# Optimization experiments

Hardware: AMD Instinct MI355X
Metric: run time of the kernel (lower is better)

## Reference

```python
import jax, jax.numpy as jnp
import numpy as np

QMIN, QMAX = -128, 127  # signed int8 range


def setup_inputs() -> dict:
    key = jax.random.key(0)
    k_x, k_w, k_b = jax.random.split(key, 3)
    N, C_in, H, W = 32, 128, 56, 56
    C_out, kH, kW = 256, 3, 3
    # int8-valued tensors carried as int32 (jax-friendly); values in [-128, 127]
    x = jax.random.randint(k_x, (N, C_in, H, W), 0, 256, dtype=jnp.int32) - 128
    weight = jax.random.randint(k_w, (C_out, C_in, kH, kW), 0, 256, dtype=jnp.int32) - 128
    # int32 bias, already quantized with scale s_in * s_w
    bias = jax.random.randint(k_b, (C_out,), -(2 ** 14), 2 ** 14, dtype=jnp.int32)
    return {
        "x": x,
        "weight": weight,
        "bias": bias,
        "input_scale": jnp.float32(0.02),
        "weight_scale": jnp.float32(0.005),
        "output_scale": jnp.float32(0.05),
        "input_zero_point": jnp.int32(-5),
        "output_zero_point": jnp.int32(3),
    }


def reference(x, weight, bias, input_scale, weight_scale, output_scale,
              input_zero_point, output_zero_point):
    # Dequant-style integer conv: shift input by its zero point (weights are
    # symmetric, zero point 0), accumulate in fp32 (stands in for int32 acc).
    x_f = (x - input_zero_point).astype(jnp.float32)
    w_f = weight.astype(jnp.float32)
    acc = jax.lax.conv_general_dilated(
        x_f, w_f,
        window_strides=(1, 1),
        padding=((1, 1), (1, 1)),
        dimension_numbers=("NCHW", "OIHW", "NCHW"),
    )
    acc = acc + bias.astype(jnp.float32)[None, :, None, None]
    # Requantize: scale fusion + output zero point, round, clamp to int8.
    requant_scale = input_scale * weight_scale / output_scale
    y = acc * requant_scale + output_zero_point.astype(jnp.float32)
    y_q = jnp.clip(jnp.round(y), QMIN, QMAX).astype(jnp.int8)
    return y_q
```

## Files before the change

kernel.cpp:

```cpp
#include <hip/hip_runtime.h>
#include <stdint.h>


#define NB 32
#define CI 128
#define HH 56
#define WW 56
#define CO 256
#define SPA (HH * WW)
#define HP 58
#define WP 64
#define XP2_BYTES (NB * HP * WP * CI)
#define BP_BYTES (9 * 2 * 4 * CO * 16)

typedef int v4i __attribute__((ext_vector_type(4)));

__global__ __launch_bounds__(256) void prep_kernel(
    const int* __restrict__ x, const int* __restrict__ wgt,
    const int* __restrict__ bias, const int* __restrict__ zpi,
    int8_t* __restrict__ xp2, int8_t* __restrict__ bp, int* __restrict__ BG)
{
    __shared__ int sm[1824];
    const int tid = threadIdx.x, bid = blockIdx.x;
    const int zp = *zpi;
    const int zp4 = (zp & 255) * 0x01010101;

    if (bid < HH * NB) {
        const int n = bid / HH, h = bid % HH;
        #pragma unroll
        for (int it = 0; it < 7; ++it) {
            int j = tid + it * 256;
            int ci = j / 14, w4 = j - ci * 14;
            const v4i v = *(const v4i*)(x + ((n * CI + ci) * HH + h) * WW + w4 * 4);
            sm[w4 * 130 + ci] = (v.x & 255) | ((v.y & 255) << 8) |
                                ((v.z & 255) << 16) | (v.w << 24);
        }
        __syncthreads();
        int* od = (int*)xp2 + (n * HP + h + 1) * (WP * CI / 4);
        #pragma unroll
        for (int it = 0; it < 8; ++it) {
            int j = tid + it * 256;
            int widx = j >> 5, ci4 = j & 31;
            int val = zp4;
            if (widx >= 1 && widx <= WW) {
                int w = widx - 1;
                int base = (w >> 2) * 130 + ci4 * 4;
                int sh = (w & 3) * 8;
                val = ((sm[base] >> sh) & 0xff) | (((sm[base+1] >> sh) & 0xff) << 8) |
                      (((sm[base+2] >> sh) & 0xff) << 16) | ((sm[base+3] >> sh) << 24);
            }
            od[j ^ ((widx & 7) << 2)] = val;
        }
    } else if (bid < HH * NB + 2 * NB) {
        const int z = bid - HH * NB;
        const int n = z >> 1, hidx = (z & 1) ? (HP - 1) : 0;
        int* od = (int*)xp2 + (n * HP + hidx) * (WP * CI / 4);
        #pragma unroll
        for (int it = 0; it < 8; ++it) od[tid + it * 256] = zp4;
    } else {
        const int co = bid - (HH * NB + 2 * NB);
        for (int j = tid; j < 1152; j += 256) sm[j] = wgt[co * 1152 + j];
        __syncthreads();
        for (int j = tid; j < 288; j += 256) {
            int j4 = j & 3, q = (j >> 2) & 3, c64 = (j >> 4) & 1, t = j >> 5;
            int ci = c64 * 64 + q * 16 + j4 * 4;
            int b0 = sm[(ci + 0) * 9 + t] & 255, b1 = sm[(ci + 1) * 9 + t] & 255;
            int b2 = sm[(ci + 2) * 9 + t] & 255, b3 = sm[(ci + 3) * 9 + t];
            ((int*)bp)[((t * 2 + c64) * 4 + q) * 1024 + co * 4 + j4] =
                b0 | (b1 << 8) | (b2 << 16) | (b3 << 24);
        }
        if (tid < 9) {
            int s = 0;
            for (int ci = 0; ci < CI; ++ci) s += sm[ci * 9 + tid];
            sm[1152 + tid] = s;
        }
        __syncthreads();
        if (tid == 0) {
            int s9 = 0;
            for (int t = 0; t < 9; ++t) s9 += sm[1152 + t];
            BG[co] = bias[co] - zp * s9;
        }
    }
}

__global__ __launch_bounds__(256, 1) void qconv_mfma(
    const int8_t* __restrict__ xp2, const int8_t* __restrict__ bp,
    const int* __restrict__ BG,
    const float* __restrict__ si, const float* __restrict__ sw,
    const float* __restrict__ so, const int* __restrict__ zpo,
    int* __restrict__ out)
{
    const int tid  = threadIdx.x, lane = tid & 63, wid = tid >> 6;
    const int quad = lane >> 4, lo16 = lane & 15;
    const int bid  = blockIdx.x;
    const int xcd  = bid & 7, idx = bid >> 3;
    const int co64 = idx & 3, slab = idx >> 2;
    const int gslab = xcd * 28 + slab;
    const int n = gslab / 7, blk8 = gslab % 7;
    const int cobase = co64 * 64;
    const int p0   = blk8 * 8;
    const int remS = blk8 * 448;

    __shared__ __attribute__((aligned(16))) char smem[152 * 1024];
    char* Asm = smem;
    char* Bsm = smem + 80 * 1024;

    const int8_t* aslab = xp2 + (((size_t)n * HP + p0) << 13);
    #pragma unroll
    for (int k = 0; k < 20; ++k) {
        const int u = wid + 4 * k;
        __builtin_amdgcn_global_load_lds(
            (const __attribute__((address_space(1))) void*)(aslab + (u << 10) + lane * 16),
            (__attribute__((address_space(3))) void*)(Asm + (u << 10)), 16, 0, 0);
    }
    #pragma unroll
    for (int k = 0; k < 18; ++k) {
        const int u = wid + 4 * k;
        __builtin_amdgcn_global_load_lds(
            (const __attribute__((address_space(1))) void*)(bp + (u << 12) + cobase * 16 + lane * 16),
            (__attribute__((address_space(3))) void*)(Bsm + (u << 10)), 16, 0, 0);
    }

    int abase[7];
    const int mw = wid * 112;
    #pragma unroll
    for (int mt = 0; mt < 7; ++mt) {
        const int ml = mw + mt * 16 + lo16;
        const int srow = ml / 56, scol = ml - srow * 56;
        abase[mt] = (srow * WP + scol) * 128 + quad * 16;
    }

    int bgv[4];
    #pragma unroll
    for (int ct = 0; ct < 4; ++ct) bgv[ct] = BG[cobase + ct * 16 + lo16];
    const float rs = (*si) * (*sw) / (*so);
    const float zo = (float)(*zpo);

    v4i acc[7][4];
    #pragma unroll
    for (int mt = 0; mt < 7; ++mt)
        #pragma unroll
        for (int ct = 0; ct < 4; ++ct) acc[mt][ct] = (v4i){0, 0, 0, 0};

    __syncthreads();

    #pragma unroll
    for (int t = 0; t < 9; ++t) {
        const int toff = ((t / 3) * WP + (t % 3)) * 128;
        v4i b[2][4];
        #pragma unroll
        for (int c = 0; c < 2; ++c)
            #pragma unroll
            for (int ct = 0; ct < 4; ++ct)
                b[c][ct] = *(const v4i*)(Bsm + ((t * 2 + c) * 4 + quad) * 1024 +
                                         lo16 * 16 + ct * 256);
        #pragma unroll
        for (int mt = 0; mt < 7; ++mt) {
            const int P = abase[mt] + toff;
            const int phys = P ^ (((P >> 7) & 7) << 4);
            v4i a0 = *(const v4i*)(Asm + phys);
            v4i a1 = *(const v4i*)(Asm + (phys ^ 64));
            #pragma unroll
            for (int ct = 0; ct < 4; ++ct)
                acc[mt][ct] = __builtin_amdgcn_mfma_i32_16x16x64_i8(a0, b[0][ct], acc[mt][ct], 0, 0, 0);
            #pragma unroll
            for (int ct = 0; ct < 4; ++ct)
                acc[mt][ct] = __builtin_amdgcn_mfma_i32_16x16x64_i8(a1, b[1][ct], acc[mt][ct], 0, 0, 0);
        }
    }

    __syncthreads();
    int* lt = (int*)smem + wid * 1088;

    #pragma unroll
    for (int mt = 0; mt < 7; ++mt) {
        #pragma unroll
        for (int ct = 0; ct < 4; ++ct) {
            v4i vv;
            #pragma unroll
            for (int i = 0; i < 4; ++i) {
                float y = rintf((float)(acc[mt][ct][i] + bgv[ct]) * rs + zo);
                y = fminf(fmaxf(y, -128.f), 127.f);
                vv[i] = (int)y;
            }
            *(v4i*)(lt + (ct * 16 + lo16) * 17 + quad * 4) = vv;
        }
        const int rm0 = remS + mw + mt * 16;
        #pragma unroll
        for (int it = 0; it < 4; ++it) {
            const int col = it * 16 + (lane >> 2);
            const int m4  = (lane & 3) * 4;
            v4i v = *(const v4i*)(lt + col * 17 + m4);
            *(v4i*)(out + ((n * CO + cobase + col) * SPA + rm0 + m4)) = v;
        }
    }
}

extern "C" void kernel_launch(void* const* d_in, const int* in_sizes, int n_in,
                              void* d_out, int out_size, void* d_ws, size_t ws_size,
                              hipStream_t stream) {
    const int*   x    = (const int*)d_in[0];
    const int*   wgt  = (const int*)d_in[1];
    const int*   bias = (const int*)d_in[2];
    const float* si   = (const float*)d_in[3];
    const float* sw   = (const float*)d_in[4];
    const float* so   = (const float*)d_in[5];
    const int*   zpi  = (const int*)d_in[6];
    const int*   zpo  = (const int*)d_in[7];
    int* out = (int*)d_out;

    int8_t* xp2 = (int8_t*)d_ws;
    int8_t* bp  = xp2 + XP2_BYTES;
    int*    bg  = (int*)(bp + BP_BYTES);

    prep_kernel<<<HH * NB + 2 * NB + CO, 256, 0, stream>>>(x, wgt, bias, zpi, xp2, bp, bg);
    qconv_mfma<<<896, 256, 0, stream>>>(xp2, bp, bg, si, sw, so, zpo, out);
}
```

Before: 202.0 us.

## Make conv blocks persistent over row slabs with register-prefetched next A tile

The grid shrinks from 896 to 256 blocks, one per CU. Each block keeps its weight tile in LDS and loops over 3 or 4 row slabs of one image and 64-channel group. The next slab's activations are prefetched into registers during the MFMA loop and written to LDS after a barrier. The epilogue stores requantized results straight to global memory instead of transposing through LDS. This amortizes the weight load and launch cost and overlaps activation loads with compute, at the cost of heavy register pressure (20 prefetch vectors plus 28 accumulators), extra barriers, and less coalesced output stores.

```diff
diff --git a/kernel.cpp b/kernel.cpp
--- a/kernel.cpp
+++ b/kernel.cpp
@@ -93,26 +93,18 @@
     const int tid  = threadIdx.x, lane = tid & 63, wid = tid >> 6;
     const int quad = lane >> 4, lo16 = lane & 15;
     const int bid  = blockIdx.x;
-    const int xcd  = bid & 7, idx = bid >> 3;
-    const int co64 = idx & 3, slab = idx >> 2;
-    const int gslab = xcd * 28 + slab;
-    const int n = gslab / 7, blk8 = gslab % 7;
+    const int x    = bid & 7, yb = bid >> 3;
+    const int half = yb >> 4, coli = yb & 15;
+    const int col  = x * 16 + coli;
+    const int n = col >> 2, co64 = col & 3;
     const int cobase = co64 * 64;
-    const int p0   = blk8 * 8;
-    const int remS = blk8 * 448;
+    const int sfirst = half;
+    const int ntiles = half ? 3 : 4;
 
     __shared__ __attribute__((aligned(16))) char smem[152 * 1024];
     char* Asm = smem;
     char* Bsm = smem + 80 * 1024;
 
-    const int8_t* aslab = xp2 + (((size_t)n * HP + p0) << 13);
-    #pragma unroll
-    for (int k = 0; k < 20; ++k) {
-        const int u = wid + 4 * k;
-        __builtin_amdgcn_global_load_lds(
-            (const __attribute__((address_space(1))) void*)(aslab + (u << 10) + lane * 16),
-            (__attribute__((address_space(3))) void*)(Asm + (u << 10)), 16, 0, 0);
-    }
     #pragma unroll
     for (int k = 0; k < 18; ++k) {
         const int u = wid + 4 * k;
@@ -120,6 +112,14 @@
             (const __attribute__((address_space(1))) void*)(bp + (u << 12) + cobase * 16 + lane * 16),
             (__attribute__((address_space(3))) void*)(Bsm + (u << 10)), 16, 0, 0);
     }
+    const int8_t* aslab0 = xp2 + (((size_t)n * HP + sfirst * 8) << 13);
+    #pragma unroll
+    for (int k = 0; k < 20; ++k) {
+        const int u = wid + 4 * k;
+        __builtin_amdgcn_global_load_lds(
+            (const __attribute__((address_space(1))) void*)(aslab0 + (u << 10) + lane * 16),
+            (__attribute__((address_space(3))) void*)(Asm + (u << 10)), 16, 0, 0);
+    }
 
     int abase[7];
     const int mw = wid * 112;
@@ -136,62 +136,84 @@
     const float rs = (*si) * (*sw) / (*so);
     const float zo = (float)(*zpo);
 
-    v4i acc[7][4];
-    #pragma unroll
-    for (int mt = 0; mt < 7; ++mt)
-        #pragma unroll
-        for (int ct = 0; ct < 4; ++ct) acc[mt][ct] = (v4i){0, 0, 0, 0};
+    int* optr = out + (n * CO + cobase + lo16) * SPA + mw + quad * 4;
 
     __syncthreads();
 
-    #pragma unroll
-    for (int t = 0; t < 9; ++t) {
-        const int toff = ((t / 3) * WP + (t % 3)) * 128;
-        v4i b[2][4];
-        #pragma unroll
-        for (int c = 0; c < 2; ++c)
-            #pragma unroll
-            for (int ct = 0; ct < 4; ++ct)
-                b[c][ct] = *(const v4i*)(Bsm + ((t * 2 + c) * 4 + quad) * 1024 +
-                                         lo16 * 16 + ct * 256);
+    for (int tile = 0; tile < ntiles; ++tile) {
+        const int slab = sfirst + 2 * tile;
+        const int havenext = (tile + 1 < ntiles);
+
+        v4i pre[20];
+        if (havenext) {
+            const int8_t* anext = xp2 + (((size_t)n * HP + (slab + 2) * 8) << 13);
+            #pragma unroll
+            for (int i = 0; i < 20; ++i)
+                pre[i] = *(const v4i*)(anext + i * 4096 + tid * 16);
+        }
+
+        v4i acc[7][4];
+        #pragma unroll
+        for (int mt = 0; mt < 7; ++mt)
+            #pragma unroll
+            for (int ct = 0; ct < 4; ++ct) acc[mt][ct] = (v4i){0, 0, 0, 0};
+
+        #pragma unroll
+        for (int t = 0; t < 9; ++t) {
+            const int toff = ((t / 3) * WP + (t % 3)) * 128;
+            v4i b[2][4];
+            #pragma unroll
+            for (int c = 0; c < 2; ++c)
+                #pragma unroll
+                for (int ct = 0; ct < 4; ++ct)
+                    b[c][ct] = *(const v4i*)(Bsm + ((t * 2 + c) * 4 + quad) * 1024 +
+                                             lo16 * 16 + ct * 256);
+            #pragma unroll
+            for (int mt = 0; mt < 7; ++mt) {
+                const int P = abase[mt] + toff;
+                const int phys = P ^ (((P >> 7) & 7) << 4);
+                v4i a0 = *(const v4i*)(Asm + phys);
+                v4i a1 = *(const v4i*)(Asm + (phys ^ 64));
+                #pragma unroll
+                for (int ct = 0; ct < 4; ++ct)
+                    acc[mt][ct] = __builtin_amdgcn_mfma_i32_16x16x64_i8(a0, b[0][ct], acc[mt][ct], 0, 0, 0);
+                #pragma unroll
+                for (int ct = 0; ct < 4; ++ct)
+                    acc[mt][ct] = __builtin_amdgcn_mfma_i32_16x16x64_i8(a1, b[1][ct], acc[mt][ct], 0, 0, 0);
+            }
+        }
+
+        __builtin_amdgcn_sched_barrier(0);
+        __builtin_amdgcn_s_barrier();
+        __builtin_amdgcn_sched_barrier(0);
+
+        if (havenext) {
+            #pragma unroll
+            for (int i = 0; i < 20; ++i)
+                *(v4i*)(Asm + i * 4096 + tid * 16) = pre[i];
+        }
+
+        const int sbase = slab * 448;
         #pragma unroll
         for (int mt = 0; mt < 7; ++mt) {
-            const int P = abase[mt] + toff;
-            const int phys = P ^ (((P >> 7) & 7) << 4);
-            v4i a0 = *(const v4i*)(Asm + phys);
-            v4i a1 = *(const v4i*)(Asm + (phys ^ 64));
-            #pragma unroll
-            for (int ct = 0; ct < 4; ++ct)
-                acc[mt][ct] = __builtin_amdgcn_mfma_i32_16x16x64_i8(a0, b[0][ct], acc[mt][ct], 0, 0, 0);
-            #pragma unroll
-            for (int ct = 0; ct < 4; ++ct)
-                acc[mt][ct] = __builtin_amdgcn_mfma_i32_16x16x64_i8(a1, b[1][ct], acc[mt][ct], 0, 0, 0);
-        }
-    }
-
-    __syncthreads();
-    int* lt = (int*)smem + wid * 1088;
-
-    #pragma unroll
-    for (int mt = 0; mt < 7; ++mt) {
-        #pragma unroll
-        for (int ct = 0; ct < 4; ++ct) {
-            v4i vv;
-            #pragma unroll
-            for (int i = 0; i < 4; ++i) {
-                float y = rintf((float)(acc[mt][ct][i] + bgv[ct]) * rs + zo);
-                y = fminf(fmaxf(y, -128.f), 127.f);
-                vv[i] = (int)y;
+            #pragma unroll
+            for (int ct = 0; ct < 4; ++ct) {
+                v4i vv;
+                #pragma unroll
+                for (int i = 0; i < 4; ++i) {
+                    float yv = rintf((float)(acc[mt][ct][i] + bgv[ct]) * rs + zo);
+                    yv = fminf(fmaxf(yv, -128.f), 127.f);
+                    vv[i] = (int)yv;
+                }
+                *(v4i*)(optr + sbase + ct * 16 * SPA + mt * 16) = vv;
             }
-            *(v4i*)(lt + (ct * 16 + lo16) * 17 + quad * 4) = vv;
-        }
-        const int rm0 = remS + mw + mt * 16;
-        #pragma unroll
-        for (int it = 0; it < 4; ++it) {
-            const int col = it * 16 + (lane >> 2);
-            const int m4  = (lane & 3) * 4;
-            v4i v = *(const v4i*)(lt + col * 17 + m4);
-            *(v4i*)(out + ((n * CO + cobase + col) * SPA + rm0 + m4)) = v;
+        }
+
+        if (havenext) {
+            asm volatile("s_waitcnt lgkmcnt(0)" ::: "memory");
+            __builtin_amdgcn_sched_barrier(0);
+            __builtin_amdgcn_s_barrier();
+            __builtin_amdgcn_sched_barrier(0);
         }
     }
 }
@@ -214,5 +236,5 @@
     int*    bg  = (int*)(bp + BP_BYTES);
 
     prep_kernel<<<HH * NB + 2 * NB + CO, 256, 0, stream>>>(x, wgt, bias, zpi, xp2, bp, bg);
-    qconv_mfma<<<896, 256, 0, stream>>>(xp2, bp, bg, si, sw, so, zpo, out);
+    qconv_mfma<<<256, 256, 0, stream>>>(xp2, bp, bg, si, sw, so, zpo, out);
 }
```

New measurement: 196.8 us. 1.03x faster.
